# Kernel tuning notes

Hardware: AMD Instinct MI355X
Metric: run time of the kernel (lower is better)

Reference implementation:

```python
import jax, jax.numpy as jnp
import numpy as np
import math

D_MODEL = 1024
N_HEADS = 16
D_K = D_MODEL // N_HEADS
B, S = 2, 2048


def setup_inputs() -> dict:
    key = jax.random.key(0)
    ks = jax.random.split(key, 11)
    sc = 1.0 / math.sqrt(D_MODEL)
    inp = {
        'q': jax.random.normal(ks[0], (B, S, D_MODEL), jnp.float32),
        'k': jax.random.normal(ks[1], (B, S, D_MODEL), jnp.float32),
        'v': jax.random.normal(ks[2], (B, S, D_MODEL), jnp.float32),
        'mask': jnp.tril(jnp.ones((S, S), jnp.int32))[None, None],  # [1,1,S,S] causal
        'W_q': jax.random.normal(ks[3], (D_MODEL, D_MODEL), jnp.float32) * sc,
        'b_q': jnp.zeros((D_MODEL,), jnp.float32),
        'W_k': jax.random.normal(ks[4], (D_MODEL, D_MODEL), jnp.float32) * sc,
        'b_k': jnp.zeros((D_MODEL,), jnp.float32),
        'W_v': jax.random.normal(ks[5], (D_MODEL, D_MODEL), jnp.float32) * sc,
        'b_v': jnp.zeros((D_MODEL,), jnp.float32),
        'W_o': jax.random.normal(ks[6], (D_MODEL, D_MODEL), jnp.float32) * sc,
        'b_o': jnp.zeros((D_MODEL,), jnp.float32),
    }
    return inp


def reference(q, k, v, mask, W_q, b_q, W_k, b_k, W_v, b_v, W_o, b_o):
    # Linear projections then split heads: [B,S,D] -> [B,H,S,d_k]
    def split_heads(x):
        b, s, _ = x.shape
        return x.reshape(b, s, N_HEADS, D_K).transpose(0, 2, 1, 3)

    Q = split_heads(q @ W_q + b_q)
    K = split_heads(k @ W_k + b_k)
    V = split_heads(v @ W_v + b_v)

    scores = jnp.einsum('bhqd,bhkd->bhqk', Q, K) / math.sqrt(D_K)
    scores = jnp.where(mask == 0, jnp.float32(-1e9), scores)
    attn = jax.nn.softmax(scores, axis=-1)  # dropout is identity in eval mode
    out = jnp.einsum('bhqk,bhkd->bhqd', attn, V)
    out = out.transpose(0, 2, 1, 3).reshape(q.shape[0], -1, D_MODEL)
    return out @ W_o + b_o
```

## Files before the change

### kernel.cpp

```cpp
#include <hip/hip_runtime.h>
#include <hip/hip_bf16.h>

#define D_MODEL 1024
#define S_LEN   2048
#define BATCH   2
#define NH      16
#define DK      64

typedef __bf16 bf16_t;
typedef __attribute__((ext_vector_type(8))) __bf16 bf16x8;
typedef __attribute__((ext_vector_type(4))) float f32x4;

#if __has_builtin(__builtin_amdgcn_exp2f)
#define EXP2F(x) __builtin_amdgcn_exp2f(x)
#else
#define EXP2F(x) exp2f(x)
#endif

#define Q_SCALE 0.1803368801111204f

#define GLDS16(gp, lp) __builtin_amdgcn_global_load_lds( \
    (const __attribute__((address_space(1))) void*)(gp), \
    (__attribute__((address_space(3))) void*)(lp), 16, 0, 0)

__global__ __launch_bounds__(256) void prep(
    const float* __restrict__ q, const float* __restrict__ k, const float* __restrict__ v,
    const float* __restrict__ Wq, const float* __restrict__ Wk,
    const float* __restrict__ Wv, const float* __restrict__ Wo,
    bf16_t* __restrict__ qkvb, bf16_t* __restrict__ WqkvT, bf16_t* __restrict__ WoT)
{
    __shared__ float t[32][33];
    const int tid = threadIdx.x;
    if (blockIdx.z < 3) {
        const long NELEM = (long)BATCH * S_LEN * D_MODEL;
        const float* src = (blockIdx.z == 0) ? q : (blockIdx.z == 1) ? k : v;
        long i = ((long)blockIdx.x * 256 + tid) * 8;
        float4 a = *(const float4*)(src + i);
        float4 b = *(const float4*)(src + i + 4);
        bf16x8 o;
        o[0] = (bf16_t)a.x; o[1] = (bf16_t)a.y; o[2] = (bf16_t)a.z; o[3] = (bf16_t)a.w;
        o[4] = (bf16_t)b.x; o[5] = (bf16_t)b.y; o[6] = (bf16_t)b.z; o[7] = (bf16_t)b.w;
        *(bf16x8*)(qkvb + blockIdx.z * NELEM + i) = o;
    } else {
        int wz = (blockIdx.z - 3) * 2048 + blockIdx.x;
        int mat = wz >> 10;
        int tile = wz & 1023;
        int bx = tile & 31, by = tile >> 5;
        const float* in = (mat == 0) ? Wq : (mat == 1) ? Wk : (mat == 2) ? Wv : Wo;
        bf16_t* out = (mat < 3) ? (WqkvT + (long)mat * D_MODEL * D_MODEL) : WoT;
        int tx = tid & 31, ty = tid >> 5;
        int gx = bx * 32, gy = by * 32;
#pragma unroll
        for (int i = 0; i < 32; i += 8)
            t[ty + i][tx] = in[(gy + ty + i) * D_MODEL + gx + tx];
        __syncthreads();
#pragma unroll
        for (int i = 0; i < 32; i += 8)
            out[(gx + ty + i) * D_MODEL + gy + tx] = (bf16_t)t[tx][ty + i];
    }
}

#define BM 128
#define BN 128
#define BKT 64

template <int ROWS>
__device__ __forceinline__ void stage_swz(const bf16_t* __restrict__ G, int row0,
                                          int k0, bf16_t* __restrict__ Ls, int tid) {
#pragma unroll
    for (int it = 0; it < ROWS / 32; ++it) {
        int g = it * 256 + tid;
        int row = g >> 3;
        int c = (g & 7) ^ (row & 7);
        GLDS16(&G[(long)(row0 + row) * D_MODEL + k0 + c * 8],
               &Ls[(it * 256 + (tid & ~63)) * 8]);
    }
}

__device__ __forceinline__ bf16x8 frag_swz(const bf16_t* __restrict__ Ls, int row, int cg) {
    return *(const bf16x8*)(&Ls[(row * 8 + (cg ^ (row & 7))) * 8]);
}

#define QM 64
constexpr int QKV_SMEM = (QM * BKT + BN * BKT);
__global__ __launch_bounds__(256) void gemm_qkv(
    const bf16_t* __restrict__ qkvb, const bf16_t* __restrict__ WqkvT,
    const float* __restrict__ bq, const float* __restrict__ bk, const float* __restrict__ bv,
    bf16_t* __restrict__ Qw, bf16_t* __restrict__ Kw, bf16_t* __restrict__ Vt)
{
    __shared__ __align__(16) bf16_t smem[QKV_SMEM];
    bf16_t* As = smem;
    bf16_t* Bs = smem + QM * BKT;
    const int z = blockIdx.z;
    const bf16_t* A  = qkvb + (long)z * BATCH * S_LEN * D_MODEL;
    const bf16_t* BT = WqkvT + (long)z * D_MODEL * D_MODEL;
    const float* bias = (z == 0) ? bq : (z == 1) ? bk : bv;
    bf16_t* Cb = (z == 0) ? Qw : (z == 1) ? Kw : Vt;
    const float oscale = (z == 0) ? Q_SCALE : 1.0f;

    const int tid  = threadIdx.x;
    const int wave = tid >> 6, lane = tid & 63;
    const int lrow = lane & 15, kgrp = lane >> 4;
    const int wm = (wave >> 1) * 32, wn = (wave & 1) * 64;
    int lin = blockIdx.y * 8 + blockIdx.x;
    int m0 = (lin & 63) * QM;
    int n0 = (lin >> 6) * BN;

    f32x4 acc[2][4] = {};

    for (int k0 = 0; k0 < D_MODEL; k0 += BKT) {
        stage_swz<QM>(A, m0, k0, As, tid);
        stage_swz<BN>(BT, n0, k0, Bs, tid);
        __syncthreads();
#pragma unroll
        for (int kk = 0; kk < 2; ++kk) {
            bf16x8 af[2], bfr[4];
#pragma unroll
            for (int mi = 0; mi < 2; ++mi)
                af[mi] = frag_swz(As, wm + mi * 16 + lrow, kk * 4 + kgrp);
#pragma unroll
            for (int ni = 0; ni < 4; ++ni)
                bfr[ni] = frag_swz(Bs, wn + ni * 16 + lrow, kk * 4 + kgrp);
#pragma unroll
            for (int mi = 0; mi < 2; ++mi)
#pragma unroll
                for (int ni = 0; ni < 4; ++ni)
                    acc[mi][ni] = __builtin_amdgcn_mfma_f32_16x16x32_bf16(af[mi], bfr[ni], acc[mi][ni], 0, 0, 0);
        }
        __syncthreads();
    }

    if (z != 2) {
#pragma unroll
        for (int mi = 0; mi < 2; ++mi)
#pragma unroll
            for (int ni = 0; ni < 4; ++ni) {
                int col = n0 + wn + ni * 16 + lrow;
                float bvf = bias[col];
#pragma unroll
                for (int r = 0; r < 4; ++r) {
                    int row = m0 + wm + mi * 16 + kgrp * 4 + r;
                    float vv = (acc[mi][ni][r] + bvf) * oscale;
                    int b = row >> 11, s = row & (S_LEN - 1);
                    int h = col >> 6, d = col & (DK - 1);
                    Cb[(((long)(b * NH + h) * S_LEN + s) * DK) + d] = (bf16_t)vv;
                }
            }
    } else {
        bf16_t* Ct = smem;
#pragma unroll
        for (int mi = 0; mi < 2; ++mi)
#pragma unroll
            for (int ni = 0; ni < 4; ++ni) {
                int cl = wn + ni * 16 + lrow;
                float bvf = bias[n0 + cl];
#pragma unroll
                for (int r = 0; r < 4; ++r) {
                    int rl = wm + mi * 16 + kgrp * 4 + r;
                    Ct[cl * 72 + rl] = (bf16_t)(acc[mi][ni][r] + bvf);
                }
            }
        __syncthreads();
        const int b = m0 >> 11, sbase = m0 & (S_LEN - 1);
#pragma unroll
        for (int pass = 0; pass < 4; ++pass) {
            int dl = pass * 32 + (tid >> 3);
            int sc = (tid & 7) * 8;
            int colg = n0 + dl;
            int h = colg >> 6, d = colg & (DK - 1);
            bf16_t* dst = Cb + (((long)(b * NH + h) * DK + d) * S_LEN + sbase + sc);
            *(bf16x8*)(dst) = *(const bf16x8*)&Ct[dl * 72 + sc];
        }
    }
}

#define OM 64
__global__ __launch_bounds__(256) void gemm_out(
    const bf16_t* __restrict__ A, const bf16_t* __restrict__ BT,
    const float* __restrict__ bias, float* __restrict__ Cf)
{
    __shared__ __align__(16) bf16_t As[OM * BKT];
    __shared__ __align__(16) bf16_t Bs[BN * BKT];
    const int tid  = threadIdx.x;
    const int wave = tid >> 6, lane = tid & 63;
    const int lrow = lane & 15, kgrp = lane >> 4;
    const int wm = (wave >> 1) * 32, wn = (wave & 1) * 64;
    int lin = blockIdx.y * 8 + blockIdx.x;
    int m0 = (lin & 63) * OM;
    int n0 = (lin >> 6) * BN;

    f32x4 acc[2][4] = {};

    for (int k0 = 0; k0 < D_MODEL; k0 += BKT) {
        stage_swz<OM>(A, m0, k0, As, tid);
        stage_swz<BN>(BT, n0, k0, Bs, tid);
        __syncthreads();
#pragma unroll
        for (int kk = 0; kk < 2; ++kk) {
            bf16x8 af[2], bfr[4];
#pragma unroll
            for (int mi = 0; mi < 2; ++mi)
                af[mi] = frag_swz(As, wm + mi * 16 + lrow, kk * 4 + kgrp);
#pragma unroll
            for (int ni = 0; ni < 4; ++ni)
                bfr[ni] = frag_swz(Bs, wn + ni * 16 + lrow, kk * 4 + kgrp);
#pragma unroll
            for (int mi = 0; mi < 2; ++mi)
#pragma unroll
                for (int ni = 0; ni < 4; ++ni)
                    acc[mi][ni] = __builtin_amdgcn_mfma_f32_16x16x32_bf16(af[mi], bfr[ni], acc[mi][ni], 0, 0, 0);
        }
        __syncthreads();
    }

#pragma unroll
    for (int mi = 0; mi < 2; ++mi)
#pragma unroll
        for (int ni = 0; ni < 4; ++ni) {
            int col = n0 + wn + ni * 16 + lrow;
            float bvf = bias[col];
#pragma unroll
            for (int r = 0; r < 4; ++r) {
                int row = m0 + wm + mi * 16 + kgrp * 4 + r;
                Cf[(long)row * D_MODEL + col] = acc[mi][ni][r] + bvf;
            }
        }
}

__device__ __forceinline__ int krow_perm(int r) {
    return ((r >> 5) + 2 * ((r >> 2) & 1)) * 16 + ((r >> 3) & 3) * 4 + (r & 3);
}

__device__ __forceinline__ void attn_one_qtile(
    int qi, int bh, int wave, int lrow, int kgrp,
    int r0, int c0, int r1,
    const bf16_t* __restrict__ Qh, const bf16_t* __restrict__ Kh,
    const bf16_t* __restrict__ Vth, bf16_t* __restrict__ O,
    bf16_t* __restrict__ Ks, bf16_t* __restrict__ Vs)
{
    const int q0 = qi * 64;
    const int qrow = q0 + wave * 16;
    const int qg = qrow + lrow;

    bf16x8 qf[2];
#pragma unroll
    for (int kk = 0; kk < 2; ++kk)
        qf[kk] = *(const bf16x8*)(&Qh[(qrow + lrow) * DK + kk * 32 + kgrp * 8]);

    f32x4 acc[4] = {};
    float lsum = 0.f;

    const int nt = qi + 1;
    const int rr0 = krow_perm(r0), rr1 = krow_perm(r1);

    uint4 kpre0 = *(const uint4*)(&Kh[(long)r0 * DK + c0]);
    uint4 kpre1 = *(const uint4*)(&Kh[(long)r1 * DK + c0]);
    uint4 vpre0 = *(const uint4*)(&Vth[(long)r0 * S_LEN + c0]);
    uint4 vpre1 = *(const uint4*)(&Vth[(long)r1 * S_LEN + c0]);

    for (int t = 0; t < nt; ++t) {
        __syncthreads();
        *(uint4*)(&Ks[rr0 * 72 + c0]) = kpre0;
        *(uint4*)(&Ks[rr1 * 72 + c0]) = kpre1;
        *(uint4*)(&Vs[r0 * 72 + c0]) = vpre0;
        *(uint4*)(&Vs[r1 * 72 + c0]) = vpre1;
        if (t + 1 < nt) {
            const int j0n = (t + 1) * 64;
            kpre0 = *(const uint4*)(&Kh[(long)(j0n + r0) * DK + c0]);
            kpre1 = *(const uint4*)(&Kh[(long)(j0n + r1) * DK + c0]);
            vpre0 = *(const uint4*)(&Vth[(long)r0 * S_LEN + j0n + c0]);
            vpre1 = *(const uint4*)(&Vth[(long)r1 * S_LEN + j0n + c0]);
        }
        __syncthreads();

        const int j0 = t * 64;

        f32x4 sc[4] = {};
#pragma unroll
        for (int kk = 0; kk < 2; ++kk)
#pragma unroll
            for (int ni = 0; ni < 4; ++ni) {
                bf16x8 kf = *(const bf16x8*)(&Ks[(ni * 16 + lrow) * 72 + kk * 32 + kgrp * 8]);
                sc[ni] = __builtin_amdgcn_mfma_f32_16x16x32_bf16(kf, qf[kk], sc[ni], 0, 0, 0);
            }

        float pb[4][4];
        const bool needmask = (j0 + 63 > qrow);
        if (needmask) {
#pragma unroll
            for (int ni = 0; ni < 4; ++ni) {
                const int cb = j0 + (ni & 1) * 32 + kgrp * 8 + ((ni >> 1) << 2);
#pragma unroll
                for (int r = 0; r < 4; ++r) {
                    float pv = EXP2F(sc[ni][r]);
                    if (cb + r > qg) pv = 0.f;
                    lsum += pv;
                    pb[ni][r] = pv;
                }
            }
        } else {
#pragma unroll
            for (int ni = 0; ni < 4; ++ni)
#pragma unroll
                for (int r = 0; r < 4; ++r) {
                    float pv = EXP2F(sc[ni][r]);
                    lsum += pv;
                    pb[ni][r] = pv;
                }
        }

        bf16x8 pf0, pf1;
#pragma unroll
        for (int r = 0; r < 4; ++r) {
            pf0[r]     = (bf16_t)pb[0][r];
            pf0[r + 4] = (bf16_t)pb[2][r];
            pf1[r]     = (bf16_t)pb[1][r];
            pf1[r + 4] = (bf16_t)pb[3][r];
        }

#pragma unroll
        for (int di = 0; di < 4; ++di) {
            bf16x8 vf = *(const bf16x8*)(&Vs[(di * 16 + lrow) * 72 + kgrp * 8]);
            acc[di] = __builtin_amdgcn_mfma_f32_16x16x32_bf16(pf0, vf, acc[di], 0, 0, 0);
        }
#pragma unroll
        for (int di = 0; di < 4; ++di) {
            bf16x8 vf = *(const bf16x8*)(&Vs[(di * 16 + lrow) * 72 + 32 + kgrp * 8]);
            acc[di] = __builtin_amdgcn_mfma_f32_16x16x32_bf16(pf1, vf, acc[di], 0, 0, 0);
        }
    }

    lsum += __shfl_xor(lsum, 16);
    lsum += __shfl_xor(lsum, 32);

    const int b = bh >> 4, h = bh & (NH - 1);
#pragma unroll
    for (int r = 0; r < 4; ++r) {
        float inv = 1.f / __shfl(lsum, kgrp * 4 + r);
        int s = qrow + kgrp * 4 + r;
#pragma unroll
        for (int di = 0; di < 4; ++di) {
            int d = di * 16 + lrow;
            O[((long)(b * S_LEN + s)) * D_MODEL + h * DK + d] = (bf16_t)(acc[di][r] * inv);
        }
    }
}

__global__ __launch_bounds__(256, 2) void attn_kernel(
    const bf16_t* __restrict__ Q, const bf16_t* __restrict__ K,
    const bf16_t* __restrict__ Vt, bf16_t* __restrict__ O)
{
    __shared__ __align__(16) bf16_t Ks[64 * 72];
    __shared__ __align__(16) bf16_t Vs[64 * 72];

    const int bh = blockIdx.y;
    const int p  = blockIdx.x;
    const int tid = threadIdx.x, wave = tid >> 6, lane = tid & 63;
    const int lrow = lane & 15, kgrp = lane >> 4;

    const bf16_t* Qh  = Q  + (long)bh * S_LEN * DK;
    const bf16_t* Kh  = K  + (long)bh * S_LEN * DK;
    const bf16_t* Vth = Vt + (long)bh * DK * S_LEN;

    const int f0 = tid * 8;
    const int r0 = f0 >> 6, c0 = f0 & 63;
    const int r1 = (f0 + 2048) >> 6;

    attn_one_qtile(31 - p, bh, wave, lrow, kgrp, r0, c0, r1,
                   Qh, Kh, Vth, O, Ks, Vs);
    attn_one_qtile(p, bh, wave, lrow, kgrp, r0, c0, r1,
                   Qh, Kh, Vth, O, Ks, Vs);
}

extern "C" void kernel_launch(void* const* d_in, const int* in_sizes, int n_in,
                              void* d_out, int out_size, void* d_ws, size_t ws_size,
                              hipStream_t stream) {
    const float* q  = (const float*)d_in[0];
    const float* k  = (const float*)d_in[1];
    const float* v  = (const float*)d_in[2];
    const float* Wq = (const float*)d_in[4];
    const float* bq = (const float*)d_in[5];
    const float* Wk = (const float*)d_in[6];
    const float* bk = (const float*)d_in[7];
    const float* Wv = (const float*)d_in[8];
    const float* bv = (const float*)d_in[9];
    const float* Wo = (const float*)d_in[10];
    const float* bo = (const float*)d_in[11];

    char* ws = (char*)d_ws;
    const size_t Mi = 1024 * 1024;
    bf16_t* WqkvT = (bf16_t*)(ws);
    bf16_t* WoT   = (bf16_t*)(ws + 6 * Mi);
    bf16_t* Qw    = (bf16_t*)(ws + 8 * Mi);
    bf16_t* Kw    = (bf16_t*)(ws + 16 * Mi);
    bf16_t* Vtw   = (bf16_t*)(ws + 24 * Mi);
    bf16_t* qkvb  = (bf16_t*)(ws + 32 * Mi);
    bf16_t* Aw    = (bf16_t*)(ws + 32 * Mi);

    prep<<<dim3(2048, 1, 5), 256, 0, stream>>>(q, k, v, Wq, Wk, Wv, Wo,
                                               qkvb, WqkvT, WoT);

    gemm_qkv<<<dim3(8, (BATCH * S_LEN) / QM, 3), 256, 0, stream>>>(
        qkvb, WqkvT, bq, bk, bv, Qw, Kw, Vtw);

    attn_kernel<<<dim3(16, BATCH * NH), 256, 0, stream>>>(Qw, Kw, Vtw, Aw);

    gemm_out<<<dim3(8, (BATCH * S_LEN) / OM), 256, 0, stream>>>(
        Aw, WoT, bo, (float*)d_out);
}
```

Measured before the change: 220.8 us.

## Fuse fp32-to-bf16 activation conversion into QKV GEMM staging loads

The separate pass that converted q/k/v from fp32 to bf16 into a workspace buffer is removed. The QKV GEMM now loads fp32 activations directly, converts them in registers and writes swizzled bf16 into LDS, while the weight transpose stays in its own prep kernel. This drops one full read/write pass over the activations. In exchange, each GEMM block reads twice as many bytes for A, re-reads it once per N-tile (8 times), and loses the asynchronous global-to-LDS load path for that operand.

```diff
diff --git a/kernel.cpp b/kernel.cpp
--- a/kernel.cpp
+++ b/kernel.cpp
@@ -23,44 +23,27 @@
     (const __attribute__((address_space(1))) void*)(gp), \
     (__attribute__((address_space(3))) void*)(lp), 16, 0, 0)
 
-__global__ __launch_bounds__(256) void prep(
-    const float* __restrict__ q, const float* __restrict__ k, const float* __restrict__ v,
-    const float* __restrict__ Wq, const float* __restrict__ Wk,
-    const float* __restrict__ Wv, const float* __restrict__ Wo,
-    bf16_t* __restrict__ qkvb, bf16_t* __restrict__ WqkvT, bf16_t* __restrict__ WoT)
+__global__ void prep_w(const float* __restrict__ Wq, const float* __restrict__ Wk,
+                       const float* __restrict__ Wv, const float* __restrict__ Wo,
+                       bf16_t* __restrict__ WqkvT, bf16_t* __restrict__ WoT)
 {
     __shared__ float t[32][33];
-    const int tid = threadIdx.x;
-    if (blockIdx.z < 3) {
-        const long NELEM = (long)BATCH * S_LEN * D_MODEL;
-        const float* src = (blockIdx.z == 0) ? q : (blockIdx.z == 1) ? k : v;
-        long i = ((long)blockIdx.x * 256 + tid) * 8;
-        float4 a = *(const float4*)(src + i);
-        float4 b = *(const float4*)(src + i + 4);
-        bf16x8 o;
-        o[0] = (bf16_t)a.x; o[1] = (bf16_t)a.y; o[2] = (bf16_t)a.z; o[3] = (bf16_t)a.w;
-        o[4] = (bf16_t)b.x; o[5] = (bf16_t)b.y; o[6] = (bf16_t)b.z; o[7] = (bf16_t)b.w;
-        *(bf16x8*)(qkvb + blockIdx.z * NELEM + i) = o;
-    } else {
-        int wz = (blockIdx.z - 3) * 2048 + blockIdx.x;
-        int mat = wz >> 10;
-        int tile = wz & 1023;
-        int bx = tile & 31, by = tile >> 5;
-        const float* in = (mat == 0) ? Wq : (mat == 1) ? Wk : (mat == 2) ? Wv : Wo;
-        bf16_t* out = (mat < 3) ? (WqkvT + (long)mat * D_MODEL * D_MODEL) : WoT;
-        int tx = tid & 31, ty = tid >> 5;
-        int gx = bx * 32, gy = by * 32;
-#pragma unroll
-        for (int i = 0; i < 32; i += 8)
-            t[ty + i][tx] = in[(gy + ty + i) * D_MODEL + gx + tx];
-        __syncthreads();
-#pragma unroll
-        for (int i = 0; i < 32; i += 8)
-            out[(gx + ty + i) * D_MODEL + gy + tx] = (bf16_t)t[tx][ty + i];
-    }
-}
-
-#define BM 128
+    const int mat = blockIdx.z;
+    const int tile = blockIdx.x;
+    const int bx = tile & 31, by = tile >> 5;
+    const float* in = (mat == 0) ? Wq : (mat == 1) ? Wk : (mat == 2) ? Wv : Wo;
+    bf16_t* out = (mat < 3) ? (WqkvT + (long)mat * D_MODEL * D_MODEL) : WoT;
+    int tx = threadIdx.x, ty = threadIdx.y;
+    int gx = bx * 32, gy = by * 32;
+#pragma unroll
+    for (int i = 0; i < 32; i += 8)
+        t[ty + i][tx] = in[(gy + ty + i) * D_MODEL + gx + tx];
+    __syncthreads();
+#pragma unroll
+    for (int i = 0; i < 32; i += 8)
+        out[(gx + ty + i) * D_MODEL + gy + tx] = (bf16_t)t[tx][ty + i];
+}
+
 #define BN 128
 #define BKT 64
 
@@ -77,6 +60,22 @@
     }
 }
 
+__device__ __forceinline__ void stage_cvt(const float* __restrict__ G, int row0,
+                                          int k0, bf16_t* __restrict__ Ls, int tid) {
+#pragma unroll
+    for (int it = 0; it < 2; ++it) {
+        int g = it * 256 + tid;
+        int row = g >> 3, cg = g & 7;
+        const float* src = &G[(long)(row0 + row) * D_MODEL + k0 + cg * 8];
+        float4 a = *(const float4*)(src);
+        float4 b = *(const float4*)(src + 4);
+        bf16x8 o;
+        o[0] = (bf16_t)a.x; o[1] = (bf16_t)a.y; o[2] = (bf16_t)a.z; o[3] = (bf16_t)a.w;
+        o[4] = (bf16_t)b.x; o[5] = (bf16_t)b.y; o[6] = (bf16_t)b.z; o[7] = (bf16_t)b.w;
+        *(bf16x8*)(&Ls[(row * 8 + (cg ^ (row & 7))) * 8]) = o;
+    }
+}
+
 __device__ __forceinline__ bf16x8 frag_swz(const bf16_t* __restrict__ Ls, int row, int cg) {
     return *(const bf16x8*)(&Ls[(row * 8 + (cg ^ (row & 7))) * 8]);
 }
@@ -84,7 +83,8 @@
 #define QM 64
 constexpr int QKV_SMEM = (QM * BKT + BN * BKT);
 __global__ __launch_bounds__(256) void gemm_qkv(
-    const bf16_t* __restrict__ qkvb, const bf16_t* __restrict__ WqkvT,
+    const float* __restrict__ qsrc, const float* __restrict__ ksrc,
+    const float* __restrict__ vsrc, const bf16_t* __restrict__ WqkvT,
     const float* __restrict__ bq, const float* __restrict__ bk, const float* __restrict__ bv,
     bf16_t* __restrict__ Qw, bf16_t* __restrict__ Kw, bf16_t* __restrict__ Vt)
 {
@@ -92,7 +92,7 @@
     bf16_t* As = smem;
     bf16_t* Bs = smem + QM * BKT;
     const int z = blockIdx.z;
-    const bf16_t* A  = qkvb + (long)z * BATCH * S_LEN * D_MODEL;
+    const float* A   = (z == 0) ? qsrc : (z == 1) ? ksrc : vsrc;
     const bf16_t* BT = WqkvT + (long)z * D_MODEL * D_MODEL;
     const float* bias = (z == 0) ? bq : (z == 1) ? bk : bv;
     bf16_t* Cb = (z == 0) ? Qw : (z == 1) ? Kw : Vt;
@@ -109,8 +109,8 @@
     f32x4 acc[2][4] = {};
 
     for (int k0 = 0; k0 < D_MODEL; k0 += BKT) {
-        stage_swz<QM>(A, m0, k0, As, tid);
         stage_swz<BN>(BT, n0, k0, Bs, tid);
+        stage_cvt(A, m0, k0, As, tid);
         __syncthreads();
 #pragma unroll
         for (int kk = 0; kk < 2; ++kk) {
@@ -394,14 +394,13 @@
     bf16_t* Qw    = (bf16_t*)(ws + 8 * Mi);
     bf16_t* Kw    = (bf16_t*)(ws + 16 * Mi);
     bf16_t* Vtw   = (bf16_t*)(ws + 24 * Mi);
-    bf16_t* qkvb  = (bf16_t*)(ws + 32 * Mi);
     bf16_t* Aw    = (bf16_t*)(ws + 32 * Mi);
 
-    prep<<<dim3(2048, 1, 5), 256, 0, stream>>>(q, k, v, Wq, Wk, Wv, Wo,
-                                               qkvb, WqkvT, WoT);
+    dim3 tb(32, 8);
+    prep_w<<<dim3(1024, 1, 4), tb, 0, stream>>>(Wq, Wk, Wv, Wo, WqkvT, WoT);
 
     gemm_qkv<<<dim3(8, (BATCH * S_LEN) / QM, 3), 256, 0, stream>>>(
-        qkvb, WqkvT, bq, bk, bv, Qw, Kw, Vtw);
+        q, k, v, WqkvT, bq, bk, bv, Qw, Kw, Vtw);
 
     attn_kernel<<<dim3(16, BATCH * NH), 256, 0, stream>>>(Qw, Kw, Vtw, Aw);
 
```

New measurement: 219.9 us. No clear change (-0.4%).
